# Kernel optimization log

Measured on AMD Instinct MI355X. Metric: run time of the kernel, lower is better.

## Reference

```python
import jax, jax.numpy as jnp
import numpy as np


def _adder2d(x, w, stride, padding):
    """AdderNet 'convolution': out[b,o,i,j] = -sum_p |patch[b,p,i,j] - w[o,p]|.

    x: [B, C, H, W], w: [O, C, kh, kw]. Patches are extracted in (C, kh, kw)
    channel-major order, matching torch.nn.functional.unfold / w.reshape(O, -1).
    """
    O, C, kh, kw = w.shape
    patches = jax.lax.conv_general_dilated_patches(
        x, (kh, kw), (stride, stride), [(padding, padding), (padding, padding)])
    B, P, Ho, Wo = patches.shape  # P = C*kh*kw
    p = patches.reshape(B, P, Ho * Wo)
    wf = w.reshape(O, P)

    def per_out(wo):  # sequential over small O to avoid a [B,O,P,L] blowup
        return -jnp.sum(jnp.abs(p - wo[None, :, None]), axis=1)  # [B, L]

    out = jax.lax.map(per_out, wf)  # [O, B, L]
    return jnp.transpose(out, (1, 0, 2)).reshape(B, O, Ho, Wo)


def setup_inputs() -> dict:
    key = jax.random.key(0)
    ks = jax.random.split(key, 5)
    x = jax.random.normal(ks[0], (4096, 1, 28, 28), dtype=jnp.float32)
    w1 = jax.random.normal(ks[1], (16, 1, 3, 3), dtype=jnp.float32)
    w2 = jax.random.normal(ks[2], (32, 16, 3, 3), dtype=jnp.float32)
    w3 = jax.random.normal(ks[3], (16, 32, 3, 3), dtype=jnp.float32)
    w4 = jax.random.normal(ks[4], (10, 16, 3, 3), dtype=jnp.float32)
    return {"x": x, "w1": w1, "w2": w2, "w3": w3, "w4": w4}


def reference(x, w1, w2, w3, w4):
    h = x - 0.5
    h = jax.nn.relu((_adder2d(h, w1, 2, 0) + 10.0) / 4.0)   # [B,16,13,13]
    h = jax.nn.relu((_adder2d(h, w2, 2, 1) + 130.0) / 8.0)  # [B,32,7,7]
    h = jax.nn.relu((_adder2d(h, w3, 2, 1) + 280.0) / 16.0)  # [B,16,4,4]
    h = _adder2d(h, w4, 2, 0)                                # [B,10,1,1]
    h = h.reshape(h.shape[0], -1)                            # [B,10]
    return jax.nn.log_softmax(h, axis=1)
```

## Files before the change

### kernel.cpp

```cpp
#include <hip/hip_runtime.h>
#include <math.h>


#if defined(__has_builtin)
#if __has_builtin(__builtin_amdgcn_sad_u16)
#define HAS_SAD 1
#endif
#endif

__device__ __forceinline__ unsigned sadu16(unsigned a, unsigned b, unsigned acc) {
#ifdef HAS_SAD
  return __builtin_amdgcn_sad_u16(a, b, acc);
#else
  int al = (int)(a & 0xFFFFu), ah = (int)(a >> 16);
  int bl = (int)(b & 0xFFFFu), bh = (int)(b >> 16);
  return acc + (unsigned)(al > bl ? al - bl : bl - al)
             + (unsigned)(ah > bh ? ah - bh : bh - ah);
#endif
}

__device__ __forceinline__ unsigned quant(float v) {
  return (unsigned)fmaf(v, 1024.0f, 8192.5f);
}
__device__ __forceinline__ unsigned quantx(float v) {
  return (unsigned)fmaf(v, 1024.0f, 7680.5f);
}
__device__ __forceinline__ int imax(int a, int b) { return a > b ? a : b; }

#define QPAD 0x20002000u

__global__ void adder_prep(const float* __restrict__ w1, const float* __restrict__ w2,
                           const float* __restrict__ w3, const float* __restrict__ w4,
                           unsigned* __restrict__ qw) {
  int k = blockIdx.x * 256 + threadIdx.x;
  if (k < 96) {
    int o = k / 6, r = k % 6, kh = r >> 1, h = r & 1;
    const float* p = w1 + o * 9 + kh * 3;
    qw[k] = h ? quant(p[2]) : (quant(p[0]) | (quant(p[1]) << 16));
  } else if (k < 2400) {
    int k2 = k - 96, m = k2 / 288, r = k2 % 288, o = r / 9, pk = r % 9;
    int s = o * 144 + 2 * m * 9 + pk;
    qw[k] = quant(w2[s]) | (quant(w2[s + 9]) << 16);
  } else if (k < 4704) {
    int k3 = k - 2400, m2 = k3 / 144, r = k3 % 144, o = r / 9, pk = r % 9;
    int s = o * 288 + 2 * m2 * 9 + pk;
    qw[k] = quant(w3[s]) | (quant(w3[s + 9]) << 16);
  } else if (k < 5424) {
    int k4 = k - 4704, m = k4 / 90, r = k4 % 90, o = r / 9, pk = r % 9;
    int s = o * 144 + 2 * m * 9 + pk;
    qw[k] = quant(w4[s]) | (quant(w4[s + 9]) << 16);
  }
}

__global__ __launch_bounds__(64, 3) void adder_main(
    const float* __restrict__ gx,
    const unsigned* __restrict__ qw,
    float* __restrict__ gout)
{
  __shared__ __align__(16) unsigned sA1[1800];
  __shared__ __align__(16) unsigned sA2[1296];

  const int t = threadIdx.x;
  const int b = blockIdx.x;
  const float* img = gx + (size_t)b * 784;

  for (int k = t; k < 448; k += 64) {
    int plane = k / 56, c = k % 56;
    int y, x;
    if (c < 15)      { y = 0;      x = c; }
    else if (c < 30) { y = 14;     x = c - 15; }
    else if (c < 43) { y = c - 29; x = 0; }
    else             { y = c - 42; x = 14; }
    sA1[plane * 225 + y * 15 + x] = QPAD;
  }
  for (int k = t; k < 512; k += 64) {
    int plane = k >> 5, c = k & 31;
    int y, x;
    if (c < 9)       { y = 0; x = c; }
    else if (c < 18) { y = 8; x = c - 9; }
    else if (c < 25) { y = c - 17; x = 0; }
    else             { y = c - 24; x = 8; }
    sA2[plane * 81 + y * 9 + x] = QPAD;
  }

  if (t < 52) {
    const int i = t >> 2, jq = t & 3;
    unsigned r[3][5], mw[3][4];
#pragma unroll
    for (int kh = 0; kh < 3; ++kh) {
      const float* rp = img + (2 * i + kh) * 28 + 8 * jq;
      float4 A = *(const float4*)(rp);
      float4 B = *(const float4*)(rp + 4);
      float2 C = *(const float2*)(rp + 8);
      r[kh][0] = quantx(A.x) | (quantx(A.y) << 16);
      r[kh][1] = quantx(A.z) | (quantx(A.w) << 16);
      r[kh][2] = quantx(B.x) | (quantx(B.y) << 16);
      r[kh][3] = quantx(B.z) | (quantx(B.w) << 16);
      r[kh][4] = quantx(C.x) | (quantx(C.y) << 16);
#pragma unroll
      for (int c = 0; c < 4; ++c) mw[kh][c] = r[kh][c + 1] & 0xFFFFu;
    }
#pragma unroll 1
    for (int op = 0; op < 8; ++op) {
      const unsigned* w = qw + op * 12;
      unsigned a0[4], a1[4];
#pragma unroll
      for (int jj = 0; jj < 4; ++jj) { a0[jj] = 0u; a1[jj] = 0u; }
#pragma unroll
      for (int kh = 0; kh < 3; ++kh) {
        unsigned wa01 = w[kh * 2], wa2 = w[kh * 2 + 1];
        unsigned wb01 = w[6 + kh * 2], wb2 = w[6 + kh * 2 + 1];
#pragma unroll
        for (int jj = 0; jj < 4; ++jj) {
          a0[jj] = sadu16(r[kh][jj], wa01, a0[jj]);
          a0[jj] = sadu16(mw[kh][jj], wa2, a0[jj]);
          a1[jj] = sadu16(r[kh][jj], wb01, a1[jj]);
          a1[jj] = sadu16(mw[kh][jj], wb2, a1[jj]);
        }
      }
      unsigned* dst = sA1 + op * 225 + (i + 1) * 15 + 4 * jq + 1;
#pragma unroll
      for (int jj = 0; jj < 4; ++jj) {
        if (4 * jq + jj < 13) {
          int q0 = imax(10752 - (int)((a0[jj] + 2u) >> 2), 8192);
          int q1 = imax(10752 - (int)((a1[jj] + 2u) >> 2), 8192);
          dst[jj] = (unsigned)q0 | ((unsigned)q1 << 16);
        }
      }
    }
  }
  __syncthreads();

  if (t < 49) {
    const int i = t / 7, j = t % 7;
    unsigned acc[32];
#pragma unroll
    for (int o = 0; o < 32; ++o) acc[o] = 0u;
    const unsigned* qw2 = qw + 96;
#pragma unroll 1
    for (int m = 0; m < 8; ++m) {
      const unsigned* plane = sA1 + m * 225 + 2 * j;
      unsigned p[3][3];
#pragma unroll
      for (int kh = 0; kh < 3; ++kh)
#pragma unroll
        for (int c = 0; c < 3; ++c)
          p[kh][c] = plane[(2 * i + kh) * 15 + c];
      const unsigned* wm = qw2 + m * 288;
#pragma unroll
      for (int o = 0; o < 32; ++o) {
        const unsigned* w9 = wm + o * 9;
        unsigned a = acc[o];
#pragma unroll
        for (int kh = 0; kh < 3; ++kh)
#pragma unroll
          for (int c = 0; c < 3; ++c)
            a = sadu16(p[kh][c], w9[kh * 3 + c], a);
        acc[o] = a;
      }
    }
#pragma unroll
    for (int m2 = 0; m2 < 16; ++m2) {
      int q0 = imax(24832 - (int)((acc[2 * m2] + 4u) >> 3), 8192);
      int q1 = imax(24832 - (int)((acc[2 * m2 + 1] + 4u) >> 3), 8192);
      sA2[m2 * 81 + (i + 1) * 9 + (j + 1)] = (unsigned)q0 | ((unsigned)q1 << 16);
    }
  }
  __syncthreads();

  {
    const int pos = t & 15, og = (t >> 4) & 1, mg = t >> 5;
    const int i = pos >> 2, j = pos & 3;
    unsigned acc[8];
#pragma unroll
    for (int o = 0; o < 8; ++o) acc[o] = 0u;
    const unsigned* qw3 = qw + 2400;
#pragma unroll 1
    for (int mm = 0; mm < 8; ++mm) {
      const int m2 = mg * 8 + mm;
      const unsigned* plane = sA2 + m2 * 81 + 2 * j;
      unsigned p[3][3];
#pragma unroll
      for (int kh = 0; kh < 3; ++kh)
#pragma unroll
        for (int c = 0; c < 3; ++c)
          p[kh][c] = plane[(2 * i + kh) * 9 + c];
      const unsigned* ws = qw3 + m2 * 144 + og * 72;
#pragma unroll
      for (int oo = 0; oo < 8; ++oo) {
        const unsigned* w9 = ws + oo * 9;
        unsigned a = acc[oo];
#pragma unroll
        for (int kh = 0; kh < 3; ++kh)
#pragma unroll
          for (int c = 0; c < 3; ++c)
            a = sadu16(p[kh][c], w9[kh * 3 + c], a);
        acc[oo] = a;
      }
    }
    unsigned* pp = sA1 + t * 12;
    *(uint4*)(pp)     = make_uint4(acc[0], acc[1], acc[2], acc[3]);
    *(uint4*)(pp + 4) = make_uint4(acc[4], acc[5], acc[6], acc[7]);
  }
  __syncthreads();

  if (t < 16) {
    const int pos = t;
#pragma unroll
    for (int m = 0; m < 8; ++m) {
      const int og = m >> 2, oo = 2 * (m & 3);
      const int b0 = (og * 16 + pos) * 12;
      unsigned s0 = sA1[b0 + oo]     + sA1[b0 + 384 + oo];
      unsigned s1 = sA1[b0 + oo + 1] + sA1[b0 + 384 + oo + 1];
      int q0 = imax(26112 - (int)((s0 + 8u) >> 4), 8192);
      int q1 = imax(26112 - (int)((s1 + 8u) >> 4), 8192);
      sA1[800 + m * 17 + pos] = (unsigned)q0 | ((unsigned)q1 << 16);
    }
  }
  __syncthreads();

  if (t < 40) {
    const int o = t % 10, mq = t / 10;
    const unsigned* qw4 = qw + 4704;
    unsigned acc = 0u;
#pragma unroll
    for (int mm = 0; mm < 2; ++mm) {
      const int m = mq * 2 + mm;
      const unsigned* a3 = sA1 + 800 + m * 17;
      const unsigned* w9 = qw4 + (m * 10 + o) * 9;
#pragma unroll
      for (int kh = 0; kh < 3; ++kh)
#pragma unroll
        for (int kw = 0; kw < 3; ++kw)
          acc = sadu16(a3[kh * 4 + kw], w9[kh * 3 + kw], acc);
    }
    sA1[940 + t] = acc;
  }
  __syncthreads();
  if (t < 10) {
    unsigned s = sA1[940 + t] + sA1[950 + t] + sA1[960 + t] + sA1[970 + t];
    ((float*)sA1)[980 + t] = -(float)s * (1.0f / 1024.0f);
  }
  __syncthreads();
  if (t < 10) {
    const float* lg = (const float*)sA1 + 980;
    float mx = lg[0];
#pragma unroll
    for (int k = 1; k < 10; ++k) mx = fmaxf(mx, lg[k]);
    float sum = 0.0f;
#pragma unroll
    for (int k = 0; k < 10; ++k) sum += __expf(lg[k] - mx);
    gout[(size_t)b * 10 + t] = lg[t] - mx - __logf(sum);
  }
}

extern "C" void kernel_launch(void* const* d_in, const int* in_sizes, int n_in,
                              void* d_out, int out_size, void* d_ws, size_t ws_size,
                              hipStream_t stream) {
  const float* x  = (const float*)d_in[0];
  const float* w1 = (const float*)d_in[1];
  const float* w2 = (const float*)d_in[2];
  const float* w3 = (const float*)d_in[3];
  const float* w4 = (const float*)d_in[4];
  unsigned* qw = (unsigned*)d_ws;
  float* out = (float*)d_out;
  adder_prep<<<22, 256, 0, stream>>>(w1, w2, w3, w4, qw);
  adder_main<<<4096, 64, 0, stream>>>(x, qw, out);
}
```

Before: 117.2 us.

## Use two wavefronts per image, splitting output channels across waves

Each block now runs 128 threads (two waves), and every layer's output channels are split between them. Each wave does half the layer-1 planes, 16 of the 32 layer-2 outputs, and 8 of the 16 layer-3 outputs, which halves register accumulators and per-wave serial work. The layer-3 reduction is reorganised so all 128 threads sum partials, and the layer-1 activation buffer gets a padded row stride of 19 and plane stride of 285, likely to reduce LDS bank conflicts. The cost is more shared memory per block and larger blocks, which may lower how many images are resident per CU.

```diff
diff --git a/kernel.cpp b/kernel.cpp
--- a/kernel.cpp
+++ b/kernel.cpp
@@ -28,6 +28,8 @@
 __device__ __forceinline__ int imax(int a, int b) { return a > b ? a : b; }
 
 #define QPAD 0x20002000u
+#define A1STRIDE 19
+#define A1PLANE 285
 
 __global__ void adder_prep(const float* __restrict__ w1, const float* __restrict__ w2,
                            const float* __restrict__ w3, const float* __restrict__ w4,
@@ -52,28 +54,30 @@
   }
 }
 
-__global__ __launch_bounds__(64, 3) void adder_main(
+__global__ __launch_bounds__(128, 4) void adder_main(
     const float* __restrict__ gx,
     const unsigned* __restrict__ qw,
     float* __restrict__ gout)
 {
-  __shared__ __align__(16) unsigned sA1[1800];
+  __shared__ __align__(16) unsigned sA1[2280];
   __shared__ __align__(16) unsigned sA2[1296];
 
   const int t = threadIdx.x;
+  const int l = t & 63;
+  const int wu = __builtin_amdgcn_readfirstlane(t >> 6);
   const int b = blockIdx.x;
   const float* img = gx + (size_t)b * 784;
 
-  for (int k = t; k < 448; k += 64) {
+  for (int k = t; k < 448; k += 128) {
     int plane = k / 56, c = k % 56;
     int y, x;
     if (c < 15)      { y = 0;      x = c; }
     else if (c < 30) { y = 14;     x = c - 15; }
     else if (c < 43) { y = c - 29; x = 0; }
     else             { y = c - 42; x = 14; }
-    sA1[plane * 225 + y * 15 + x] = QPAD;
-  }
-  for (int k = t; k < 512; k += 64) {
+    sA1[plane * A1PLANE + y * A1STRIDE + x] = QPAD;
+  }
+  for (int k = t; k < 512; k += 128) {
     int plane = k >> 5, c = k & 31;
     int y, x;
     if (c < 9)       { y = 0; x = c; }
@@ -83,8 +87,8 @@
     sA2[plane * 81 + y * 9 + x] = QPAD;
   }
 
-  if (t < 52) {
-    const int i = t >> 2, jq = t & 3;
+  if (l < 52) {
+    const int i = l >> 2, jq = l & 3;
     unsigned r[3][5], mw[3][4];
 #pragma unroll
     for (int kh = 0; kh < 3; ++kh) {
@@ -101,7 +105,8 @@
       for (int c = 0; c < 4; ++c) mw[kh][c] = r[kh][c + 1] & 0xFFFFu;
     }
 #pragma unroll 1
-    for (int op = 0; op < 8; ++op) {
+    for (int opp = 0; opp < 4; ++opp) {
+      const int op = wu * 4 + opp;
       const unsigned* w = qw + op * 12;
       unsigned a0[4], a1[4];
 #pragma unroll
@@ -118,7 +123,7 @@
           a1[jj] = sadu16(mw[kh][jj], wb2, a1[jj]);
         }
       }
-      unsigned* dst = sA1 + op * 225 + (i + 1) * 15 + 4 * jq + 1;
+      unsigned* dst = sA1 + op * A1PLANE + (i + 1) * A1STRIDE + 4 * jq + 1;
 #pragma unroll
       for (int jj = 0; jj < 4; ++jj) {
         if (4 * jq + jj < 13) {
@@ -131,24 +136,24 @@
   }
   __syncthreads();
 
-  if (t < 49) {
-    const int i = t / 7, j = t % 7;
-    unsigned acc[32];
-#pragma unroll
-    for (int o = 0; o < 32; ++o) acc[o] = 0u;
-    const unsigned* qw2 = qw + 96;
+  if (l < 49) {
+    const int i = l / 7, j = l % 7;
+    unsigned acc[16];
+#pragma unroll
+    for (int o = 0; o < 16; ++o) acc[o] = 0u;
+    const unsigned* qw2 = qw + 96 + wu * 144;
 #pragma unroll 1
     for (int m = 0; m < 8; ++m) {
-      const unsigned* plane = sA1 + m * 225 + 2 * j;
+      const unsigned* plane = sA1 + m * A1PLANE + 2 * j;
       unsigned p[3][3];
 #pragma unroll
       for (int kh = 0; kh < 3; ++kh)
 #pragma unroll
         for (int c = 0; c < 3; ++c)
-          p[kh][c] = plane[(2 * i + kh) * 15 + c];
+          p[kh][c] = plane[(2 * i + kh) * A1STRIDE + c];
       const unsigned* wm = qw2 + m * 288;
 #pragma unroll
-      for (int o = 0; o < 32; ++o) {
+      for (int o = 0; o < 16; ++o) {
         const unsigned* w9 = wm + o * 9;
         unsigned a = acc[o];
 #pragma unroll
@@ -160,24 +165,24 @@
       }
     }
 #pragma unroll
-    for (int m2 = 0; m2 < 16; ++m2) {
+    for (int m2 = 0; m2 < 8; ++m2) {
       int q0 = imax(24832 - (int)((acc[2 * m2] + 4u) >> 3), 8192);
       int q1 = imax(24832 - (int)((acc[2 * m2 + 1] + 4u) >> 3), 8192);
-      sA2[m2 * 81 + (i + 1) * 9 + (j + 1)] = (unsigned)q0 | ((unsigned)q1 << 16);
+      sA2[(wu * 8 + m2) * 81 + (i + 1) * 9 + (j + 1)] = (unsigned)q0 | ((unsigned)q1 << 16);
     }
   }
   __syncthreads();
 
   {
-    const int pos = t & 15, og = (t >> 4) & 1, mg = t >> 5;
+    const int pos = l & 15, g = l >> 4;
     const int i = pos >> 2, j = pos & 3;
     unsigned acc[8];
 #pragma unroll
     for (int o = 0; o < 8; ++o) acc[o] = 0u;
-    const unsigned* qw3 = qw + 2400;
+    const unsigned* qw3 = qw + 2400 + wu * 72;
 #pragma unroll 1
-    for (int mm = 0; mm < 8; ++mm) {
-      const int m2 = mg * 8 + mm;
+    for (int mm = 0; mm < 4; ++mm) {
+      const int m2 = g * 4 + mm;
       const unsigned* plane = sA2 + m2 * 81 + 2 * j;
       unsigned p[3][3];
 #pragma unroll
@@ -185,7 +190,7 @@
 #pragma unroll
         for (int c = 0; c < 3; ++c)
           p[kh][c] = plane[(2 * i + kh) * 9 + c];
-      const unsigned* ws = qw3 + m2 * 144 + og * 72;
+      const unsigned* ws = qw3 + m2 * 144;
 #pragma unroll
       for (int oo = 0; oo < 8; ++oo) {
         const unsigned* w9 = ws + oo * 9;
@@ -198,24 +203,25 @@
         acc[oo] = a;
       }
     }
-    unsigned* pp = sA1 + t * 12;
-    *(uint4*)(pp)     = make_uint4(acc[0], acc[1], acc[2], acc[3]);
-    *(uint4*)(pp + 4) = make_uint4(acc[4], acc[5], acc[6], acc[7]);
-  }
-  __syncthreads();
-
-  if (t < 16) {
-    const int pos = t;
-#pragma unroll
-    for (int m = 0; m < 8; ++m) {
-      const int og = m >> 2, oo = 2 * (m & 3);
-      const int b0 = (og * 16 + pos) * 12;
-      unsigned s0 = sA1[b0 + oo]     + sA1[b0 + 384 + oo];
-      unsigned s1 = sA1[b0 + oo + 1] + sA1[b0 + 384 + oo + 1];
-      int q0 = imax(26112 - (int)((s0 + 8u) >> 4), 8192);
-      int q1 = imax(26112 - (int)((s1 + 8u) >> 4), 8192);
-      sA1[800 + m * 17 + pos] = (unsigned)q0 | ((unsigned)q1 << 16);
-    }
+#pragma unroll
+    for (int oo = 0; oo < 8; ++oo)
+      sA1[oo * 128 + g * 32 + wu * 16 + pos] = acc[oo];
+  }
+  __syncthreads();
+
+  {
+    const int m = t >> 4, pos = t & 15;
+    const int ww = m >> 2;
+    const int oo0 = 2 * m - ww * 8;
+    unsigned s0 = 0u, s1 = 0u;
+#pragma unroll
+    for (int g = 0; g < 4; ++g) {
+      s0 += sA1[oo0 * 128 + g * 32 + ww * 16 + pos];
+      s1 += sA1[(oo0 + 1) * 128 + g * 32 + ww * 16 + pos];
+    }
+    int q0 = imax(26112 - (int)((s0 + 8u) >> 4), 8192);
+    int q1 = imax(26112 - (int)((s1 + 8u) >> 4), 8192);
+    sA1[1040 + m * 17 + pos] = (unsigned)q0 | ((unsigned)q1 << 16);
   }
   __syncthreads();
 
@@ -226,7 +232,7 @@
 #pragma unroll
     for (int mm = 0; mm < 2; ++mm) {
       const int m = mq * 2 + mm;
-      const unsigned* a3 = sA1 + 800 + m * 17;
+      const unsigned* a3 = sA1 + 1040 + m * 17;
       const unsigned* w9 = qw4 + (m * 10 + o) * 9;
 #pragma unroll
       for (int kh = 0; kh < 3; ++kh)
@@ -234,16 +240,16 @@
         for (int kw = 0; kw < 3; ++kw)
           acc = sadu16(a3[kh * 4 + kw], w9[kh * 3 + kw], acc);
     }
-    sA1[940 + t] = acc;
+    sA1[1176 + t] = acc;
   }
   __syncthreads();
   if (t < 10) {
-    unsigned s = sA1[940 + t] + sA1[950 + t] + sA1[960 + t] + sA1[970 + t];
-    ((float*)sA1)[980 + t] = -(float)s * (1.0f / 1024.0f);
+    unsigned s = sA1[1176 + t] + sA1[1186 + t] + sA1[1196 + t] + sA1[1206 + t];
+    ((float*)sA1)[1216 + t] = -(float)s * (1.0f / 1024.0f);
   }
   __syncthreads();
   if (t < 10) {
-    const float* lg = (const float*)sA1 + 980;
+    const float* lg = (const float*)sA1 + 1216;
     float mx = lg[0];
 #pragma unroll
     for (int k = 1; k < 10; ++k) mx = fmaxf(mx, lg[k]);
@@ -265,5 +271,5 @@
   unsigned* qw = (unsigned*)d_ws;
   float* out = (float*)d_out;
   adder_prep<<<22, 256, 0, stream>>>(w1, w2, w3, w4, qw);
-  adder_main<<<4096, 64, 0, stream>>>(x, qw, out);
-}
+  adder_main<<<4096, 128, 0, stream>>>(x, qw, out);
+}
```

Result: faster. 108.9 us (-7.1%).
